# Kernel optimization log

Measured on AMD Instinct MI355X. Metric: run time of the kernel, lower is better.

## Reference

```python
import jax, jax.numpy as jnp
import numpy as np

# ---- geometry constants (from init_kwargs) ----
GRID = (160, 160, 160)
ORIGIN = np.array([-160.0, -160.0, -160.0], dtype=np.float32)   # corner of image volume (mm)
VOXSIZE = np.array([2.0, 2.0, 2.0], dtype=np.float32)           # mm
TIME_RES = 300.0   # ps (FWHM-like timing resolution)
TOF_BIN = 10.0     # ps
C_HALF = 0.15      # speed of light / 2 in mm/ps -> converts TOF time to position along LOR
NSTEPS = 256       # fixed ray-march samples per LOR (jit-friendly surrogate for Siddon stepping)
N_LORS = 100000
EPS = 1e-8

SIGMA = jnp.float32(TIME_RES * C_HALF / 2.355)  # spatial TOF sigma (mm), FWHM -> sigma
NVOX = GRID[0] * GRID[1] * GRID[2]
STRIDES = np.array([GRID[1] * GRID[2], GRID[2], 1], dtype=np.int32)


def setup_inputs() -> dict:
    key = jax.random.key(0)
    k1, k2, k3, k4, k5 = jax.random.split(key, 5)
    image = jax.random.uniform(k1, GRID, dtype=jnp.float32)
    effmap = jax.random.uniform(k2, GRID, dtype=jnp.float32) + 0.5
    # LOR endpoints on a cylinder of radius 250 mm surrounding the 320 mm FOV
    R = 250.0
    ang = jax.random.uniform(k3, (N_LORS, 2), dtype=jnp.float32) * (2.0 * np.pi)
    z = jax.random.uniform(k4, (N_LORS, 2), dtype=jnp.float32) * 300.0 - 150.0
    p0 = jnp.stack([R * jnp.cos(ang[:, 0]), R * jnp.sin(ang[:, 0]), z[:, 0]], axis=-1)
    p1 = jnp.stack([-R * jnp.cos(ang[:, 1]), -R * jnp.sin(ang[:, 1]), z[:, 1]], axis=-1)
    tof = jax.random.normal(k5, (N_LORS, 1), dtype=jnp.float32) * 100.0  # ps
    lors = jnp.concatenate([p0, p1, tof], axis=-1)  # [N,7]
    return {"image": image, "effmap": effmap, "lors": lors}


def _trace(lors):
    """Ray-march samples, flat voxel indices, and TOF-weighted per-sample lengths."""
    p0, p1, tof = lors[:, 0:3], lors[:, 3:6], lors[:, 6]
    d = p1 - p0                                   # [N,3]
    L = jnp.linalg.norm(d, axis=-1)               # [N]
    dl = L / NSTEPS                               # [N] step length (mm)
    t = (jnp.arange(NSTEPS, dtype=jnp.float32) + 0.5) / NSTEPS   # [S]
    pts = p0[:, None, :] + t[None, :, None] * d[:, None, :]      # [N,S,3]
    idx = jnp.floor((pts - ORIGIN) / VOXSIZE).astype(jnp.int32)  # [N,S,3]
    inb = jnp.all((idx >= 0) & (idx < jnp.array(GRID, dtype=jnp.int32)), axis=-1)  # [N,S]
    flat = jnp.sum(jnp.clip(idx, 0, jnp.array(GRID, dtype=jnp.int32) - 1)
                   * jnp.asarray(STRIDES), axis=-1)              # [N,S]
    # TOF Gaussian weight along the ray, centered at midpoint + tof offset
    s = (t[None, :] - 0.5) * L[:, None]           # signed distance from midpoint (mm)
    s_tof = (tof * C_HALF)[:, None]
    w = jnp.exp(-0.5 * jnp.square((s - s_tof) / SIGMA))
    w = jnp.where(inb, w, 0.0) * dl[:, None]      # [N,S] intersection-length weight
    return flat, w


def reference(image, effmap, lors):
    flat, w = _trace(lors)                        # [N,S], [N,S]
    img_flat = image.reshape(-1)
    # projection: p[n] = sum_s w[n,s] * image[voxel(n,s)]
    p = jnp.sum(jnp.take(img_flat, flat) * w, axis=1)            # [N]
    # backprojection of lor_values=p: bp[v] = sum_{n,s: voxel=v} w[n,s] * p[n]
    bp = jnp.zeros((NVOX,), dtype=image.dtype).at[flat.reshape(-1)].add(
        (p[:, None] * w).reshape(-1)).reshape(GRID)
    return image / (effmap + EPS) * bp
```

## Files before the change

kernel.cpp:

```cpp
#include <hip/hip_runtime.h>
#include <math.h>

#define NSTEPS 256
#define GRIDN  160
#define NVOX   (160 * 160 * 160)
#define NTPA   20
#define NTILES (NTPA * NTPA * NTPA)
#define NREP   8
#define ITEM_CAP (4 * 1024 * 1024)
#define MAXSEG 64

#define INV_SIGMA 0.05233333f

struct LorT { float4 a; float4 b; };

__device__ __forceinline__ bool sample_vox(
    int j, float p0x, float p0y, float p0z,
    float dx, float dy, float dz, float L, float s_tof,
    int& ix, int& iy, int& iz, float& e)
{
#pragma clang fp contract(off)
    const float t = (j + 0.5f) * (1.0f / 256.0f);
    const float px = p0x + t * dx;
    const float py = p0y + t * dy;
    const float pz = p0z + t * dz;
    const float fx = floorf((px + 160.0f) * 0.5f);
    const float fy = floorf((py + 160.0f) * 0.5f);
    const float fz = floorf((pz + 160.0f) * 0.5f);
    const bool inb = (fx >= 0.0f) & (fx < 160.0f) &
                     (fy >= 0.0f) & (fy < 160.0f) &
                     (fz >= 0.0f) & (fz < 160.0f);
    const float s = (t - 0.5f) * L;
    const float u = (s - s_tof) * INV_SIGMA;
    e = 0.5f * (u * u);
    if (inb & (e < 10.0f)) {
        ix = (int)fx; iy = (int)fy; iz = (int)fz;
        return true;
    }
    return false;
}

__device__ __forceinline__ void lor_window(
    float p0x, float p0y, float p0z, float dx, float dy, float dz,
    float L, float s_tof, int& j0, int& j1)
{
#pragma clang fp contract(off)
    const float SIGMA = (float)(45.0 / 2.355);
    const float CUTS  = 4.4721360f * SIGMA;
    const float invL = 1.0f / L;
    float t0 = 0.5f + (s_tof - CUTS) * invL;
    float t1 = 0.5f + (s_tof + CUTS) * invL;
    if (t0 > t1) { const float tmp = t0; t0 = t1; t1 = tmp; }
    const float pc[3] = {p0x, p0y, p0z};
    const float dc[3] = {dx, dy, dz};
    #pragma unroll
    for (int a = 0; a < 3; ++a) {
        if (dc[a] != 0.0f) {
            const float inv = 1.0f / dc[a];
            const float ta = (-160.0f - pc[a]) * inv;
            const float tb = ( 160.0f - pc[a]) * inv;
            t0 = fmaxf(t0, fminf(ta, tb));
            t1 = fminf(t1, fmaxf(ta, tb));
        } else if (pc[a] < -160.0f || pc[a] >= 160.0f) t1 = -1.0f;
    }
    t0 = fmaxf(t0, 0.0f);
    t1 = fminf(t1, 1.0f);
    j0 = (int)floorf(t0 * 256.0f - 0.5f) - 2;
    j1 = (int)ceilf (t1 * 256.0f - 0.5f) + 2;
    if (!(t0 <= t1)) { j0 = 0; j1 = -1; }
    j0 = max(j0, 0);
    j1 = min(j1, NSTEPS - 1);
}

__global__ __launch_bounds__(256) void emit_kernel(
    const float* __restrict__ image,
    const float* __restrict__ lors, LorT* __restrict__ lortab,
    int* __restrict__ hist8, unsigned* __restrict__ items,
    float* __restrict__ p,
    unsigned* __restrict__ seg_kr, unsigned short* __restrict__ seg_jl,
    int* __restrict__ nseg,
    int n, int phase)
{
#pragma clang fp contract(off)
    const int wave = (int)((blockIdx.x * blockDim.x + threadIdx.x) >> 6);
    const int lane = threadIdx.x & 63;
    if (wave >= n) return;
    const int rep = (int)(blockIdx.x & (NREP - 1));

    float p0x, p0y, p0z, tof, dx, dy, dz, L;
    if (phase == 0) {
        const float* l = lors + (size_t)wave * 7;
        p0x = l[0]; p0y = l[1]; p0z = l[2];
        dx = l[3] - p0x; dy = l[4] - p0y; dz = l[5] - p0z; tof = l[6];
        L = sqrtf(dx * dx + dy * dy + dz * dz);
        if (lane == 0) {
            lortab[wave].a = make_float4(p0x, p0y, p0z, tof);
            lortab[wave].b = make_float4(dx, dy, dz, L);
        }
    } else {
        const float4 A = lortab[wave].a, B = lortab[wave].b;
        p0x = A.x; p0y = A.y; p0z = A.z; tof = A.w;
        dx  = B.x; dy  = B.y; dz  = B.z; L   = B.w;
    }
    const float s_tof = tof * 0.15f;
    const float dl = L * (1.0f / 256.0f);
    int j0, j1;
    lor_window(p0x, p0y, p0z, dx, dy, dz, L, s_tof, j0, j1);
    const int nk = (j1 - j0 + 64) >> 6;

    float psum = 0.0f;
    int running = 0;
    for (int k = 0; k < nk; ++k) {
        const int j = j0 + lane + (k << 6);
        int ix, iy, iz; float e;
        const bool valid = (j <= j1) &&
            sample_vox(j, p0x, p0y, p0z, dx, dy, dz, L, s_tof, ix, iy, iz, e);
        if (phase == 0) {
            if (valid)
                psum += image[ix * 25600 + iy * 160 + iz] * (__expf(-e) * dl);
        }
        const unsigned key = valid
            ? (unsigned)((ix >> 3) * 400 + (iy >> 3) * 20 + (iz >> 3))
            : 0xFFFFFFFFu;
        const unsigned prev = __shfl_up(key, 1, 64);
        const bool chg = (lane == 0) || (prev != key);
        const unsigned long long cm = __ballot(chg);
        const unsigned long long segmask = __ballot(chg && valid);
        if (chg && valid) {
            const unsigned long long above = cm & ~((2ULL << lane) - 1ULL);
            const int nxt = above ? (__ffsll((unsigned long long)above) - 1) : 64;
            const int len = nxt - lane;
            if (phase == 0) {
                const int tr = atomicAdd(&hist8[rep * NTILES + (int)key], 1);
                if (seg_kr) {
                    const int rankb =
                        (int)__popcll(segmask & ((1ULL << lane) - 1ULL));
                    const int si = running + rankb;
                    if (si < MAXSEG) {
                        seg_kr[(size_t)wave * MAXSEG + si] =
                            ((unsigned)rep << 28) | (key << 15) | (unsigned)tr;
                        seg_jl[(size_t)wave * MAXSEG + si] =
                            (unsigned short)(((unsigned)j << 6)
                                             | (unsigned)(len - 1));
                    }
                }
            } else {
                const int slot = atomicAdd(&hist8[(int)key], 1);
                if (slot < ITEM_CAP)
                    items[slot] = ((unsigned)wave << 14) | ((unsigned)j << 6)
                                | (unsigned)(len - 1);
            }
        }
        running += (int)__popcll(segmask);
    }
    if (phase == 0) {
        #pragma unroll
        for (int off = 32; off >= 1; off >>= 1) psum += __shfl_xor(psum, off, 64);
        if (lane == 0) {
            p[wave] = psum;
            if (nseg) nseg[wave] = min(running, MAXSEG);
        }
    }
}

__global__ __launch_bounds__(256) void scatter_kernel(
    const unsigned* __restrict__ seg_kr, const unsigned short* __restrict__ seg_jl,
    const int* __restrict__ nseg, const int* __restrict__ base8,
    unsigned* __restrict__ items, int n)
{
    const long long tid = (long long)blockIdx.x * blockDim.x + threadIdx.x;
    const int lor = (int)(tid >> 6);
    const int s   = (int)(tid & 63);
    if (lor >= n) return;
    if (s >= nseg[lor]) return;
    const unsigned kr = seg_kr[(size_t)lor * MAXSEG + s];
    const unsigned jl = seg_jl[(size_t)lor * MAXSEG + s];
    const int rep  = (int)(kr >> 28);
    const int key  = (int)((kr >> 15) & 0x1FFFu);
    const int rank = (int)(kr & 0x7FFFu);
    const int slot = base8[rep * NTILES + key] + rank;
    if (slot < ITEM_CAP)
        items[slot] = ((unsigned)lor << 14) | jl;
}

__global__ __launch_bounds__(256) void reduce_kernel(
    const int* __restrict__ hist8, int* __restrict__ tot)
{
    const int k = blockIdx.x * blockDim.x + threadIdx.x;
    if (k >= NTILES) return;
    int s = 0;
    #pragma unroll
    for (int r = 0; r < NREP; ++r) s += hist8[r * NTILES + k];
    tot[k] = s;
}

__global__ __launch_bounds__(1024) void scan_kernel(
    const int* __restrict__ tot, int* __restrict__ offs)
{
    __shared__ int part[1024];
    const int t = threadIdx.x;
    const int base = t * 8;
    int loc[8]; int s = 0;
    #pragma unroll
    for (int i = 0; i < 8; ++i) {
        const int h = (base + i < NTILES) ? tot[base + i] : 0;
        loc[i] = s; s += h;
    }
    part[t] = s;
    __syncthreads();
    for (int off = 1; off < 1024; off <<= 1) {
        int v = 0;
        if (t >= off) v = part[t - off];
        __syncthreads();
        part[t] += v;
        __syncthreads();
    }
    const int excl = (t > 0) ? part[t - 1] : 0;
    #pragma unroll
    for (int i = 0; i < 8; ++i)
        if (base + i < NTILES) offs[base + i] = excl + loc[i];
    if (t == 1023) offs[NTILES] = part[1023];
}

__global__ __launch_bounds__(256) void base_kernel(
    const int* __restrict__ hist8, const int* __restrict__ offs,
    int* __restrict__ base8, int* __restrict__ cursor)
{
    const int k = blockIdx.x * blockDim.x + threadIdx.x;
    if (k >= NTILES) return;
    int b = offs[k];
    cursor[k] = b;
    #pragma unroll
    for (int r = 0; r < NREP; ++r) {
        base8[r * NTILES + k] = b;
        b += hist8[r * NTILES + k];
    }
}

__global__ __launch_bounds__(256) void tileB_kernel(
    const float* __restrict__ image, const float* __restrict__ effmap,
    const LorT* __restrict__ lortab, const int* __restrict__ offs,
    const unsigned* __restrict__ items, const float* __restrict__ p,
    float* __restrict__ out)
{
    const int b = blockIdx.x;
    const int i0 = offs[b], i1 = min(offs[b + 1], ITEM_CAP);
    const int tx0 = (b / 400) << 3, ty0 = ((b / 20) % 20) << 3, tz0 = (b % 20) << 3;
    const int t = threadIdx.x;
    if (i0 >= i1) {
        for (int v = t; v < 512; v += 256) {
            const int lx = v >> 6, ly = (v >> 3) & 7, lz = v & 7;
            out[(size_t)(tx0 + lx) * 25600 + (ty0 + ly) * 160 + (tz0 + lz)] = 0.0f;
        }
        return;
    }
    __shared__ float acc[512];
    for (int v = t; v < 512; v += 256) acc[v] = 0.0f;
    __syncthreads();
    for (int idx = i0 + t; idx < i1; idx += 256) {
        const unsigned it = items[idx];
        const int lor = (int)(it >> 14);
        const int js  = (int)((it >> 6) & 255);
        const int len = (int)(it & 63) + 1;
        const float4 A = lortab[lor].a, B = lortab[lor].b;
        const float dl = B.w * (1.0f / 256.0f);
        const float s_tof = A.w * 0.15f;
        const float pv = p[lor];
        for (int m = 0; m < len; ++m) {
            int ix, iy, iz; float e;
            if (sample_vox(js + m, A.x, A.y, A.z, B.x, B.y, B.z, B.w, s_tof,
                           ix, iy, iz, e)) {
                const int lx = ix - tx0, ly = iy - ty0, lz = iz - tz0;
                if ((unsigned)lx < 8u && (unsigned)ly < 8u && (unsigned)lz < 8u)
                    atomicAdd(&acc[(lx << 6) | (ly << 3) | lz],
                              pv * (__expf(-e) * dl));
            }
        }
    }
    __syncthreads();
    for (int v = t; v < 512; v += 256) {
        const int lx = v >> 6, ly = (v >> 3) & 7, lz = v & 7;
        const size_t g = (size_t)(tx0 + lx) * 25600 + (ty0 + ly) * 160 + (tz0 + lz);
        out[g] = image[g] / (effmap[g] + 1e-8f) * acc[v];
    }
}

__global__ __launch_bounds__(256) void trace_direct_kernel(
    const float* __restrict__ image, const float* __restrict__ lors,
    float* __restrict__ bp, int n_lors)
{
#pragma clang fp contract(off)
    const int wave = (int)((blockIdx.x * blockDim.x + threadIdx.x) >> 6);
    const int lane = threadIdx.x & 63;
    if (wave >= n_lors) return;
    const float* l = lors + (size_t)wave * 7;
    const float p0x = l[0], p0y = l[1], p0z = l[2];
    const float dx = l[3] - p0x, dy = l[4] - p0y, dz = l[5] - p0z;
    const float tof = l[6];
    const float L  = sqrtf(dx * dx + dy * dy + dz * dz);
    const float dl = L * (1.0f / 256.0f);
    const float s_tof = tof * 0.15f;
    int j0, j1;
    lor_window(p0x, p0y, p0z, dx, dy, dz, L, s_tof, j0, j1);
    const int nk = (j1 - j0 + 64) >> 6;
    if (nk <= 0) return;
    int flat[4]; float w[4]; float psum = 0.0f;
    for (int k = 0; k < nk; ++k) {
        const int j = j0 + lane + (k << 6);
        int ix, iy, iz; float e; float wk = 0.0f; int fl = 0;
        if (j <= j1 &&
            sample_vox(j, p0x, p0y, p0z, dx, dy, dz, L, s_tof, ix, iy, iz, e)) {
            wk = __expf(-e) * dl;
            fl = ix * 25600 + iy * 160 + iz;
            psum += image[fl] * wk;
        }
        flat[k] = fl; w[k] = wk;
    }
    #pragma unroll
    for (int off = 32; off >= 1; off >>= 1) psum += __shfl_xor(psum, off, 64);
    for (int k = 0; k < nk; ++k)
        if (w[k] > 0.0f) atomicAdd(&bp[flat[k]], psum * w[k]);
}

__global__ __launch_bounds__(256) void finalize_kernel(
    const float4* __restrict__ image, const float4* __restrict__ effmap,
    float4* __restrict__ out, int n4)
{
    const int i = blockIdx.x * blockDim.x + threadIdx.x;
    if (i >= n4) return;
    const float4 im = image[i];
    const float4 ef = effmap[i];
    float4 b = out[i];
    b.x = im.x / (ef.x + 1e-8f) * b.x;
    b.y = im.y / (ef.y + 1e-8f) * b.y;
    b.z = im.z / (ef.z + 1e-8f) * b.z;
    b.w = im.w / (ef.w + 1e-8f) * b.w;
    out[i] = b;
}

extern "C" void kernel_launch(void* const* d_in, const int* in_sizes, int n_in,
                              void* d_out, int out_size, void* d_ws, size_t ws_size,
                              hipStream_t stream) {
    const float* image  = (const float*)d_in[0];
    const float* effmap = (const float*)d_in[1];
    const float* lors   = (const float*)d_in[2];
    float* out = (float*)d_out;
    const int n = in_sizes[2] / 7;

    char* ws = (char*)d_ws;
    const size_t hist_off   = 0;
    const size_t base_off   = hist_off + (size_t)NREP * NTILES * 4;
    const size_t tot_off    = base_off + (size_t)NREP * NTILES * 4;
    const size_t offs_off   = tot_off + 32768;
    const size_t cursor_off = offs_off + 32768;
    const size_t p_off      = cursor_off + 32768;
    const size_t lortab_off = p_off + (((size_t)n * 4 + 255) & ~(size_t)255);
    const size_t nseg_off   = lortab_off + (size_t)n * sizeof(LorT);
    const size_t kr_off     = nseg_off + (((size_t)n * 4 + 255) & ~(size_t)255);
    const size_t jl_off     = kr_off + (((size_t)n * MAXSEG * 4 + 255) & ~(size_t)255);
    const size_t items_off  = jl_off + (((size_t)n * MAXSEG * 2 + 255) & ~(size_t)255);
    const size_t total_stg  = items_off + (size_t)ITEM_CAP * 4;
    const size_t items_off2 = nseg_off;
    const size_t total_nostg = items_off2 + (size_t)ITEM_CAP * 4;

    const int tileGrid = (NTILES + 255) / 256;

    if (ws_size >= total_stg && n > 0 && n < (1 << 17)) {
        int*      hist8  = (int*)(ws + hist_off);
        int*      base8  = (int*)(ws + base_off);
        int*      tot    = (int*)(ws + tot_off);
        int*      offs   = (int*)(ws + offs_off);
        int*      cursor = (int*)(ws + cursor_off);
        float*    p      = (float*)(ws + p_off);
        LorT*     lortab = (LorT*)(ws + lortab_off);
        int*      nseg   = (int*)(ws + nseg_off);
        unsigned* seg_kr = (unsigned*)(ws + kr_off);
        unsigned short* seg_jl = (unsigned short*)(ws + jl_off);
        unsigned* items  = (unsigned*)(ws + items_off);

        hipMemsetAsync(hist8, 0, (size_t)NREP * NTILES * sizeof(int), stream);

        const int blocksE = (n + 3) / 4;
        emit_kernel<<<blocksE, 256, 0, stream>>>(image, lors, lortab, hist8, items,
                                                 p, seg_kr, seg_jl, nseg, n, 0);
        reduce_kernel<<<tileGrid, 256, 0, stream>>>(hist8, tot);
        scan_kernel<<<1, 1024, 0, stream>>>(tot, offs);
        base_kernel<<<tileGrid, 256, 0, stream>>>(hist8, offs, base8, cursor);
        const long long nthr = (long long)n * MAXSEG;
        scatter_kernel<<<(int)((nthr + 255) / 256), 256, 0, stream>>>(
            seg_kr, seg_jl, nseg, base8, items, n);
        tileB_kernel<<<NTILES, 256, 0, stream>>>(image, effmap, lortab, offs, items,
                                                 p, out);
    } else if (ws_size >= total_nostg && n > 0 && n < (1 << 17)) {
        int*      hist8  = (int*)(ws + hist_off);
        int*      base8  = (int*)(ws + base_off);
        int*      tot    = (int*)(ws + tot_off);
        int*      offs   = (int*)(ws + offs_off);
        int*      cursor = (int*)(ws + cursor_off);
        float*    p      = (float*)(ws + p_off);
        LorT*     lortab = (LorT*)(ws + lortab_off);
        unsigned* items  = (unsigned*)(ws + items_off2);

        hipMemsetAsync(hist8, 0, (size_t)NREP * NTILES * sizeof(int), stream);

        const int blocksE = (n + 3) / 4;
        emit_kernel<<<blocksE, 256, 0, stream>>>(image, lors, lortab, hist8, items,
                                                 p, nullptr, nullptr, nullptr, n, 0);
        reduce_kernel<<<tileGrid, 256, 0, stream>>>(hist8, tot);
        scan_kernel<<<1, 1024, 0, stream>>>(tot, offs);
        base_kernel<<<tileGrid, 256, 0, stream>>>(hist8, offs, base8, cursor);
        emit_kernel<<<blocksE, 256, 0, stream>>>(image, lors, lortab, cursor, items,
                                                 p, nullptr, nullptr, nullptr, n, 1);
        tileB_kernel<<<NTILES, 256, 0, stream>>>(image, effmap, lortab, offs, items,
                                                 p, out);
    } else {
        hipMemsetAsync(out, 0, (size_t)NVOX * sizeof(float), stream);
        if (n > 0)
            trace_direct_kernel<<<(n + 3) / 4, 256, 0, stream>>>(image, lors, out, n);
        const int n4 = NVOX / 4;
        finalize_kernel<<<(n4 + 255) / 256, 256, 0, stream>>>(
            (const float4*)image, (const float4*)effmap, (float4*)out, n4);
    }
}
```

Baseline: 208.0 us.

## Cache per-sample voxel index and fp16 weight in emit, consume in tile backprojection

The emit kernel now stores each valid sample's local voxel index and its TOF weight as fp16, packed into a per-LOR sample buffer. The scatter kernel copies the LOR projection value next to each item. A new tile kernel reads these cached samples instead of re-marching the ray and recomputing exp weights, so the second-pass recomputation is replaced by memory reads. The cost is about 100MB of extra sample writes and reads, and storing weights as fp16 loses precision in the backprojection. This path is used only when the workspace is large enough.

```diff
diff --git a/kernel.cpp b/kernel.cpp
--- a/kernel.cpp
+++ b/kernel.cpp
@@ -1,4 +1,5 @@
 #include <hip/hip_runtime.h>
+#include <hip/hip_fp16.h>
 #include <math.h>
 
 #define NSTEPS 256
@@ -78,7 +79,7 @@
     int* __restrict__ hist8, unsigned* __restrict__ items,
     float* __restrict__ p,
     unsigned* __restrict__ seg_kr, unsigned short* __restrict__ seg_jl,
-    int* __restrict__ nseg,
+    int* __restrict__ nseg, unsigned* __restrict__ samples,
     int n, int phase)
 {
 #pragma clang fp contract(off)
@@ -116,8 +117,18 @@
         const bool valid = (j <= j1) &&
             sample_vox(j, p0x, p0y, p0z, dx, dy, dz, L, s_tof, ix, iy, iz, e);
         if (phase == 0) {
-            if (valid)
-                psum += image[ix * 25600 + iy * 160 + iz] * (__expf(-e) * dl);
+            if (valid) {
+                const float w = __expf(-e) * dl;
+                psum += image[ix * 25600 + iy * 160 + iz] * w;
+                if (samples) {
+                    const unsigned lidx = (unsigned)((ix & 7) << 6)
+                                        | (unsigned)((iy & 7) << 3)
+                                        | (unsigned)(iz & 7);
+                    const unsigned hb =
+                        (unsigned)__half_as_ushort(__float2half(w));
+                    samples[(size_t)wave * 256 + j] = (lidx << 16) | hb;
+                }
+            }
         }
         const unsigned key = valid
             ? (unsigned)((ix >> 3) * 400 + (iy >> 3) * 20 + (iz >> 3))
@@ -166,21 +177,25 @@
 __global__ __launch_bounds__(256) void scatter_kernel(
     const unsigned* __restrict__ seg_kr, const unsigned short* __restrict__ seg_jl,
     const int* __restrict__ nseg, const int* __restrict__ base8,
-    unsigned* __restrict__ items, int n)
+    const float* __restrict__ p,
+    unsigned* __restrict__ items, float* __restrict__ items_pv, int n)
 {
     const long long tid = (long long)blockIdx.x * blockDim.x + threadIdx.x;
     const int lor = (int)(tid >> 6);
     const int s   = (int)(tid & 63);
     if (lor >= n) return;
     if (s >= nseg[lor]) return;
+    const float pv = p[lor];
     const unsigned kr = seg_kr[(size_t)lor * MAXSEG + s];
     const unsigned jl = seg_jl[(size_t)lor * MAXSEG + s];
     const int rep  = (int)(kr >> 28);
     const int key  = (int)((kr >> 15) & 0x1FFFu);
     const int rank = (int)(kr & 0x7FFFu);
     const int slot = base8[rep * NTILES + key] + rank;
-    if (slot < ITEM_CAP)
+    if (slot < ITEM_CAP) {
         items[slot] = ((unsigned)lor << 14) | jl;
+        if (items_pv) items_pv[slot] = pv;
+    }
 }
 
 __global__ __launch_bounds__(256) void reduce_kernel(
@@ -234,6 +249,48 @@
     for (int r = 0; r < NREP; ++r) {
         base8[r * NTILES + k] = b;
         b += hist8[r * NTILES + k];
+    }
+}
+
+__global__ __launch_bounds__(256) void tileB2_kernel(
+    const float* __restrict__ image, const float* __restrict__ effmap,
+    const int* __restrict__ offs, const unsigned* __restrict__ items,
+    const float* __restrict__ items_pv, const unsigned* __restrict__ samples,
+    float* __restrict__ out)
+{
+    const int b = blockIdx.x;
+    const int i0 = offs[b], i1 = min(offs[b + 1], ITEM_CAP);
+    const int tx0 = (b / 400) << 3, ty0 = ((b / 20) % 20) << 3, tz0 = (b % 20) << 3;
+    const int t = threadIdx.x;
+    if (i0 >= i1) {
+        for (int v = t; v < 512; v += 256) {
+            const int lx = v >> 6, ly = (v >> 3) & 7, lz = v & 7;
+            out[(size_t)(tx0 + lx) * 25600 + (ty0 + ly) * 160 + (tz0 + lz)] = 0.0f;
+        }
+        return;
+    }
+    __shared__ float acc[512];
+    for (int v = t; v < 512; v += 256) acc[v] = 0.0f;
+    __syncthreads();
+    for (int idx = i0 + t; idx < i1; idx += 256) {
+        const unsigned it = items[idx];
+        const float pv = items_pv[idx];
+        const int lor = (int)(it >> 14);
+        const int js  = (int)((it >> 6) & 255);
+        const int len = (int)(it & 63) + 1;
+        const unsigned* sp = samples + (size_t)lor * 256 + js;
+        for (int m = 0; m < len; ++m) {
+            const unsigned word = sp[m];
+            const float w = __half2float(
+                __ushort_as_half((unsigned short)(word & 0xFFFFu)));
+            atomicAdd(&acc[(word >> 16) & 511u], pv * w);
+        }
+    }
+    __syncthreads();
+    for (int v = t; v < 512; v += 256) {
+        const int lx = v >> 6, ly = (v >> 3) & 7, lz = v & 7;
+        const size_t g = (size_t)(tx0 + lx) * 25600 + (ty0 + ly) * 160 + (tz0 + lz);
+        out[g] = image[g] / (effmap[g] + 1e-8f) * acc[v];
     }
 }
 
@@ -359,13 +416,16 @@
     const size_t kr_off     = nseg_off + (((size_t)n * 4 + 255) & ~(size_t)255);
     const size_t jl_off     = kr_off + (((size_t)n * MAXSEG * 4 + 255) & ~(size_t)255);
     const size_t items_off  = jl_off + (((size_t)n * MAXSEG * 2 + 255) & ~(size_t)255);
-    const size_t total_stg  = items_off + (size_t)ITEM_CAP * 4;
+    const size_t pv_off     = items_off + (size_t)ITEM_CAP * 4;
+    const size_t smp_off    = pv_off + (size_t)ITEM_CAP * 4;
+    const size_t total_A    = smp_off + (size_t)n * 256 * 4;
+    const size_t total_B    = items_off + (size_t)ITEM_CAP * 4;
     const size_t items_off2 = nseg_off;
-    const size_t total_nostg = items_off2 + (size_t)ITEM_CAP * 4;
+    const size_t total_C    = items_off2 + (size_t)ITEM_CAP * 4;
 
     const int tileGrid = (NTILES + 255) / 256;
 
-    if (ws_size >= total_stg && n > 0 && n < (1 << 17)) {
+    if (ws_size >= total_A && n > 0 && n < (1 << 17)) {
         int*      hist8  = (int*)(ws + hist_off);
         int*      base8  = (int*)(ws + base_off);
         int*      tot    = (int*)(ws + tot_off);
@@ -377,21 +437,51 @@
         unsigned* seg_kr = (unsigned*)(ws + kr_off);
         unsigned short* seg_jl = (unsigned short*)(ws + jl_off);
         unsigned* items  = (unsigned*)(ws + items_off);
+        float*    items_pv = (float*)(ws + pv_off);
+        unsigned* samples  = (unsigned*)(ws + smp_off);
 
         hipMemsetAsync(hist8, 0, (size_t)NREP * NTILES * sizeof(int), stream);
 
         const int blocksE = (n + 3) / 4;
         emit_kernel<<<blocksE, 256, 0, stream>>>(image, lors, lortab, hist8, items,
-                                                 p, seg_kr, seg_jl, nseg, n, 0);
+                                                 p, seg_kr, seg_jl, nseg, samples,
+                                                 n, 0);
         reduce_kernel<<<tileGrid, 256, 0, stream>>>(hist8, tot);
         scan_kernel<<<1, 1024, 0, stream>>>(tot, offs);
         base_kernel<<<tileGrid, 256, 0, stream>>>(hist8, offs, base8, cursor);
         const long long nthr = (long long)n * MAXSEG;
         scatter_kernel<<<(int)((nthr + 255) / 256), 256, 0, stream>>>(
-            seg_kr, seg_jl, nseg, base8, items, n);
+            seg_kr, seg_jl, nseg, base8, p, items, items_pv, n);
+        tileB2_kernel<<<NTILES, 256, 0, stream>>>(image, effmap, offs, items,
+                                                  items_pv, samples, out);
+    } else if (ws_size >= total_B && n > 0 && n < (1 << 17)) {
+        int*      hist8  = (int*)(ws + hist_off);
+        int*      base8  = (int*)(ws + base_off);
+        int*      tot    = (int*)(ws + tot_off);
+        int*      offs   = (int*)(ws + offs_off);
+        int*      cursor = (int*)(ws + cursor_off);
+        float*    p      = (float*)(ws + p_off);
+        LorT*     lortab = (LorT*)(ws + lortab_off);
+        int*      nseg   = (int*)(ws + nseg_off);
+        unsigned* seg_kr = (unsigned*)(ws + kr_off);
+        unsigned short* seg_jl = (unsigned short*)(ws + jl_off);
+        unsigned* items  = (unsigned*)(ws + items_off);
+
+        hipMemsetAsync(hist8, 0, (size_t)NREP * NTILES * sizeof(int), stream);
+
+        const int blocksE = (n + 3) / 4;
+        emit_kernel<<<blocksE, 256, 0, stream>>>(image, lors, lortab, hist8, items,
+                                                 p, seg_kr, seg_jl, nseg, nullptr,
+                                                 n, 0);
+        reduce_kernel<<<tileGrid, 256, 0, stream>>>(hist8, tot);
+        scan_kernel<<<1, 1024, 0, stream>>>(tot, offs);
+        base_kernel<<<tileGrid, 256, 0, stream>>>(hist8, offs, base8, cursor);
+        const long long nthr = (long long)n * MAXSEG;
+        scatter_kernel<<<(int)((nthr + 255) / 256), 256, 0, stream>>>(
+            seg_kr, seg_jl, nseg, base8, p, items, nullptr, n);
         tileB_kernel<<<NTILES, 256, 0, stream>>>(image, effmap, lortab, offs, items,
                                                  p, out);
-    } else if (ws_size >= total_nostg && n > 0 && n < (1 << 17)) {
+    } else if (ws_size >= total_C && n > 0 && n < (1 << 17)) {
         int*      hist8  = (int*)(ws + hist_off);
         int*      base8  = (int*)(ws + base_off);
         int*      tot    = (int*)(ws + tot_off);
@@ -405,12 +495,14 @@
 
         const int blocksE = (n + 3) / 4;
         emit_kernel<<<blocksE, 256, 0, stream>>>(image, lors, lortab, hist8, items,
-                                                 p, nullptr, nullptr, nullptr, n, 0);
+                                                 p, nullptr, nullptr, nullptr,
+                                                 nullptr, n, 0);
         reduce_kernel<<<tileGrid, 256, 0, stream>>>(hist8, tot);
         scan_kernel<<<1, 1024, 0, stream>>>(tot, offs);
         base_kernel<<<tileGrid, 256, 0, stream>>>(hist8, offs, base8, cursor);
         emit_kernel<<<blocksE, 256, 0, stream>>>(image, lors, lortab, cursor, items,
-                                                 p, nullptr, nullptr, nullptr, n, 1);
+                                                 p, nullptr, nullptr, nullptr,
+                                                 nullptr, n, 1);
         tileB_kernel<<<NTILES, 256, 0, stream>>>(image, effmap, lortab, offs, items,
                                                  p, out);
     } else {
```

Result: slower. 214.4 us (+3.1%).
